# Optimization experiments

Hardware: AMD Instinct MI355X
Metric: run time of the kernel (lower is better)

Reference implementation:

```python
import jax, jax.numpy as jnp
import numpy as np

EPS = 1e-6
LOSS_WEIGHT = 1.0


def setup_inputs() -> dict:
    key = jax.random.key(0)
    k1, k2 = jax.random.split(key)
    pred = jax.random.normal(k1, (32, 2048, 2), dtype=jnp.float32)
    target = jax.random.normal(k2, (32, 2048, 2), dtype=jnp.float32)
    return {"pred": pred, "target": target}


def reference(pred, target):
    # Pairwise distances: [B, N1, N2]
    diff = pred[:, :, None, :] - target[:, None, :, :]
    sq = jnp.sum(diff * diff, axis=-1)
    dist = jnp.sqrt(sq + EPS)
    # Bidirectional Chamfer per batch item: [B]
    forward_chamfer = jnp.mean(jnp.min(dist, axis=2), axis=1)
    backward_chamfer = jnp.mean(jnp.min(dist, axis=1), axis=1)
    chamfer = forward_chamfer + backward_chamfer
    # reduction='mean' over batch -> scalar, scaled by loss_weight
    return LOSS_WEIGHT * jnp.mean(chamfer)
```

## Files before the change

### kernel.cpp

```cpp
#include <hip/hip_runtime.h>
#include <math.h>
#include <float.h>

#define B 32
#define N 2048
#define EPS 1e-6f
#define T1 256
#define Q 4
#define QBLK (T1 * Q)
#define CHUNK 128
#define C 16
#define NQ_TOTAL (2 * B * N)

__global__ __launch_bounds__(256, 8) void chamfer_min_kernel(
    const float* __restrict__ pred, const float* __restrict__ target,
    float* __restrict__ pmin) {
  const int c  = blockIdx.x;
  const int qg = blockIdx.y;
  const int db = qg >> 1;
  const int half = qg & 1;
  const int dir = db >> 5;
  const int b   = db & 31;

  const float* qraw = (dir ? target : pred) + (size_t)b * N * 2;
  const float* rraw = (dir ? pred : target) + (size_t)b * N * 2;

  __shared__ float Lf[3 * CHUNK];

  if (threadIdx.x < CHUNK) {
    const float2 rv = ((const float2*)rraw)[c * CHUNK + threadIdx.x];
    const int g = threadIdx.x >> 2, e = threadIdx.x & 3;
    Lf[12 * g + e]     = -2.f * rv.x;
    Lf[12 * g + 4 + e] = -2.f * rv.y;
    Lf[12 * g + 8 + e] = fmaf(rv.x, rv.x, rv.y * rv.y);
  }

  float qx[Q], qy[Q], m[Q];
#pragma unroll
  for (int k = 0; k < Q; ++k) {
    const float2 qp = ((const float2*)qraw)[half * QBLK + k * T1 + threadIdx.x];
    qx[k] = qp.x;
    qy[k] = qp.y;
    m[k] = FLT_MAX;
  }
  __syncthreads();

#pragma unroll 4
  for (int jj = 0; jj < CHUNK / 4; ++jj) {
    const float4 X  = *(const float4*)(Lf + 12 * jj);
    const float4 Y  = *(const float4*)(Lf + 12 * jj + 4);
    const float4 Cr = *(const float4*)(Lf + 12 * jj + 8);
#pragma unroll
    for (int k = 0; k < Q; ++k) {
      float d0 = fmaf(X.x, qx[k], fmaf(Y.x, qy[k], Cr.x));
      float d1 = fmaf(X.y, qx[k], fmaf(Y.y, qy[k], Cr.y));
      float d2 = fmaf(X.z, qx[k], fmaf(Y.z, qy[k], Cr.z));
      float d3 = fmaf(X.w, qx[k], fmaf(Y.w, qy[k], Cr.w));
      m[k] = fminf(fminf(m[k], d0), d1);
      m[k] = fminf(fminf(m[k], d2), d3);
    }
  }

#pragma unroll
  for (int k = 0; k < Q; ++k) {
    const float qq = fmaf(qx[k], qx[k], qy[k] * qy[k]);
    pmin[(size_t)c * NQ_TOTAL + qg * QBLK + k * T1 + threadIdx.x] = m[k] + qq;
  }
}

__global__ __launch_bounds__(256) void chamfer_combine_kernel(
    const float* __restrict__ pmin, float* __restrict__ partial2) {
  const int q = blockIdx.x * 256 + threadIdx.x;
  float v = FLT_MAX;
#pragma unroll
  for (int c = 0; c < C; ++c)
    v = fminf(v, pmin[(size_t)c * NQ_TOTAL + q]);
  float s = sqrtf(fmaxf(v, 0.f) + EPS);
#pragma unroll
  for (int off = 32; off > 0; off >>= 1)
    s += __shfl_down(s, off, 64);
  __shared__ float wsum[4];
  if ((threadIdx.x & 63) == 0) wsum[threadIdx.x >> 6] = s;
  __syncthreads();
  if (threadIdx.x == 0)
    partial2[blockIdx.x] = wsum[0] + wsum[1] + wsum[2] + wsum[3];
}

__global__ __launch_bounds__(512) void chamfer_final_kernel(
    const float* __restrict__ partial2, float* __restrict__ out) {
  float v = partial2[threadIdx.x];
#pragma unroll
  for (int off = 32; off > 0; off >>= 1)
    v += __shfl_down(v, off, 64);
  __shared__ float wsum[8];
  if ((threadIdx.x & 63) == 0) wsum[threadIdx.x >> 6] = v;
  __syncthreads();
  if (threadIdx.x == 0) {
    float s = 0.f;
#pragma unroll
    for (int i = 0; i < 8; ++i) s += wsum[i];
    out[0] = s * (1.0f / (float)(B * N));
  }
}

extern "C" void kernel_launch(void* const* d_in, const int* in_sizes, int n_in,
                              void* d_out, int out_size, void* d_ws, size_t ws_size,
                              hipStream_t stream) {
  const float* pred   = (const float*)d_in[0];
  const float* target = (const float*)d_in[1];
  float* out = (float*)d_out;

  float* pmin     = (float*)d_ws;
  float* partial2 = (float*)d_ws + (size_t)C * NQ_TOTAL;

  dim3 grid1(C, NQ_TOTAL / QBLK);
  chamfer_min_kernel<<<grid1, T1, 0, stream>>>(pred, target, pmin);
  chamfer_combine_kernel<<<NQ_TOTAL / 256, 256, 0, stream>>>(pmin, partial2);
  chamfer_final_kernel<<<1, 512, 0, stream>>>(partial2, out);
}
```

Measured before the change: 29.51 us.

## Precompute SoA reference layout in prep kernel, read uniform global loads instead of LDS

Adds a prep kernel that rewrites each reference cloud into a grouped SoA layout with squared norms precomputed. The min kernel then reads reference points from global memory at a wave-uniform address (readfirstlane) instead of staging them through shared memory, which removes the LDS fill and the barrier. The -2 scaling moves onto the query side. This costs an extra kernel launch and a global round trip for the expanded buffers, and the inner loop now depends on scalar/cached global loads rather than LDS broadcast reads.

```diff
diff --git a/kernel.cpp b/kernel.cpp
--- a/kernel.cpp
+++ b/kernel.cpp
@@ -10,9 +10,31 @@
 #define QBLK (T1 * Q)
 #define CHUNK 128
 #define C 16
+#define GPB 512
 #define NQ_TOTAL (2 * B * N)
 
+__global__ __launch_bounds__(256) void prep_kernel(
+    const float* __restrict__ pred, const float* __restrict__ target,
+    float* __restrict__ expPred, float* __restrict__ expTgt) {
+  const int g = blockIdx.x * 256 + threadIdx.x;
+  const int which = g >> 14;
+  const int idx = g & 16383;
+  const int b = idx >> 9, gl = idx & 511;
+
+  const float4* src = (const float4*)(which ? target : pred);
+  const float4 v0 = src[b * 1024 + 2 * gl];
+  const float4 v1 = src[b * 1024 + 2 * gl + 1];
+
+  float* dst = (which ? expTgt : expPred) + ((size_t)b * GPB + gl) * 12;
+  *(float4*)(dst)     = make_float4(v0.x, v0.z, v1.x, v1.z);
+  *(float4*)(dst + 4) = make_float4(v0.y, v0.w, v1.y, v1.w);
+  *(float4*)(dst + 8) = make_float4(
+      fmaf(v0.x, v0.x, v0.y * v0.y), fmaf(v0.z, v0.z, v0.w * v0.w),
+      fmaf(v1.x, v1.x, v1.y * v1.y), fmaf(v1.z, v1.z, v1.w * v1.w));
+}
+
 __global__ __launch_bounds__(256, 8) void chamfer_min_kernel(
+    const float* __restrict__ expPred, const float* __restrict__ expTgt,
     const float* __restrict__ pred, const float* __restrict__ target,
     float* __restrict__ pmin) {
   const int c  = blockIdx.x;
@@ -23,49 +45,41 @@
   const int b   = db & 31;
 
   const float* qraw = (dir ? target : pred) + (size_t)b * N * 2;
-  const float* rraw = (dir ? pred : target) + (size_t)b * N * 2;
+  const float* rexp = (dir ? expPred : expTgt);
 
-  __shared__ float Lf[3 * CHUNK];
+  int baseoff = (b * GPB + c * (CHUNK / 4)) * 12;
+  baseoff = __builtin_amdgcn_readfirstlane(baseoff);
+  const float* Lg = rexp + baseoff;
 
-  if (threadIdx.x < CHUNK) {
-    const float2 rv = ((const float2*)rraw)[c * CHUNK + threadIdx.x];
-    const int g = threadIdx.x >> 2, e = threadIdx.x & 3;
-    Lf[12 * g + e]     = -2.f * rv.x;
-    Lf[12 * g + 4 + e] = -2.f * rv.y;
-    Lf[12 * g + 8 + e] = fmaf(rv.x, rv.x, rv.y * rv.y);
-  }
-
-  float qx[Q], qy[Q], m[Q];
+  float qxm[Q], qym[Q], qq[Q], m[Q];
 #pragma unroll
   for (int k = 0; k < Q; ++k) {
     const float2 qp = ((const float2*)qraw)[half * QBLK + k * T1 + threadIdx.x];
-    qx[k] = qp.x;
-    qy[k] = qp.y;
+    qq[k]  = fmaf(qp.x, qp.x, qp.y * qp.y);
+    qxm[k] = -2.f * qp.x;
+    qym[k] = -2.f * qp.y;
     m[k] = FLT_MAX;
   }
-  __syncthreads();
 
 #pragma unroll 4
   for (int jj = 0; jj < CHUNK / 4; ++jj) {
-    const float4 X  = *(const float4*)(Lf + 12 * jj);
-    const float4 Y  = *(const float4*)(Lf + 12 * jj + 4);
-    const float4 Cr = *(const float4*)(Lf + 12 * jj + 8);
+    const float4 X = *(const float4*)(Lg + 12 * jj);
+    const float4 Y = *(const float4*)(Lg + 12 * jj + 4);
+    const float4 R = *(const float4*)(Lg + 12 * jj + 8);
 #pragma unroll
     for (int k = 0; k < Q; ++k) {
-      float d0 = fmaf(X.x, qx[k], fmaf(Y.x, qy[k], Cr.x));
-      float d1 = fmaf(X.y, qx[k], fmaf(Y.y, qy[k], Cr.y));
-      float d2 = fmaf(X.z, qx[k], fmaf(Y.z, qy[k], Cr.z));
-      float d3 = fmaf(X.w, qx[k], fmaf(Y.w, qy[k], Cr.w));
+      float d0 = fmaf(X.x, qxm[k], fmaf(Y.x, qym[k], R.x));
+      float d1 = fmaf(X.y, qxm[k], fmaf(Y.y, qym[k], R.y));
+      float d2 = fmaf(X.z, qxm[k], fmaf(Y.z, qym[k], R.z));
+      float d3 = fmaf(X.w, qxm[k], fmaf(Y.w, qym[k], R.w));
       m[k] = fminf(fminf(m[k], d0), d1);
       m[k] = fminf(fminf(m[k], d2), d3);
     }
   }
 
 #pragma unroll
-  for (int k = 0; k < Q; ++k) {
-    const float qq = fmaf(qx[k], qx[k], qy[k] * qy[k]);
-    pmin[(size_t)c * NQ_TOTAL + qg * QBLK + k * T1 + threadIdx.x] = m[k] + qq;
-  }
+  for (int k = 0; k < Q; ++k)
+    pmin[(size_t)c * NQ_TOTAL + qg * QBLK + k * T1 + threadIdx.x] = m[k] + qq[k];
 }
 
 __global__ __launch_bounds__(256) void chamfer_combine_kernel(
@@ -111,10 +125,13 @@
   float* out = (float*)d_out;
 
   float* pmin     = (float*)d_ws;
-  float* partial2 = (float*)d_ws + (size_t)C * NQ_TOTAL;
+  float* partial2 = pmin + (size_t)C * NQ_TOTAL;
+  float* expPred  = partial2 + 512;
+  float* expTgt   = expPred + (size_t)B * GPB * 12;
 
+  prep_kernel<<<128, 256, 0, stream>>>(pred, target, expPred, expTgt);
   dim3 grid1(C, NQ_TOTAL / QBLK);
-  chamfer_min_kernel<<<grid1, T1, 0, stream>>>(pred, target, pmin);
+  chamfer_min_kernel<<<grid1, T1, 0, stream>>>(expPred, expTgt, pred, target, pmin);
   chamfer_combine_kernel<<<NQ_TOTAL / 256, 256, 0, stream>>>(pmin, partial2);
   chamfer_final_kernel<<<1, 512, 0, stream>>>(partial2, out);
 }
```

Result: slower. 38.28 us (+29.7%).
